# Kernel optimization log

Measured on AMD Instinct MI355X. Metric: run time of the kernel, lower is better.

The kernel has to match this reference:

```python
import jax, jax.numpy as jnp
import numpy as np

B, S, T, H, VS, VT = 64, 64, 64, 1024, 32000, 32000


def _init(key, shape, scale=0.05):
    return scale * jax.random.normal(key, shape, dtype=jnp.float32)


def setup_inputs() -> dict:
    key = jax.random.key(0)
    ks = jax.random.split(key, 16)
    source = jax.random.randint(ks[0], (B, S), 0, VS)
    target = jax.random.randint(ks[1], (B, T), 0, VT)
    emb_src = _init(ks[2], (VS, H)).at[0].set(0.0)   # padding_idx=0
    emb_tgt = _init(ks[3], (VT, H)).at[0].set(0.0)   # padding_idx=0
    W_ih_enc = _init(ks[4], (4 * H, H)); W_hh_enc = _init(ks[5], (4 * H, H))
    b_ih_enc = _init(ks[6], (4 * H,));   b_hh_enc = _init(ks[7], (4 * H,))
    W_ih_dec = _init(ks[8], (4 * H, H)); W_hh_dec = _init(ks[9], (4 * H, H))
    b_ih_dec = _init(ks[10], (4 * H,));  b_hh_dec = _init(ks[11], (4 * H,))
    W_att = _init(ks[12], (H, 2 * H));   b_att = _init(ks[13], (H,))
    W_out = _init(ks[14], (VT, H));      b_out = _init(ks[15], (VT,))
    return dict(source=source, target=target, emb_src=emb_src, emb_tgt=emb_tgt,
                W_ih_enc=W_ih_enc, W_hh_enc=W_hh_enc, b_ih_enc=b_ih_enc, b_hh_enc=b_hh_enc,
                W_ih_dec=W_ih_dec, W_hh_dec=W_hh_dec, b_ih_dec=b_ih_dec, b_hh_dec=b_hh_dec,
                W_att=W_att, b_att=b_att, W_out=W_out, b_out=b_out)


def _lstm_cell(x, h, c, W_ih, W_hh, b):
    # PyTorch gate order: i, f, g, o
    gates = x @ W_ih.T + h @ W_hh.T + b
    i, f, g, o = jnp.split(gates, 4, axis=-1)
    c_new = jax.nn.sigmoid(f) * c + jax.nn.sigmoid(i) * jnp.tanh(g)
    h_new = jax.nn.sigmoid(o) * jnp.tanh(c_new)
    return h_new, c_new


def reference(source, target, emb_src, emb_tgt,
              W_ih_enc, W_hh_enc, b_ih_enc, b_hh_enc,
              W_ih_dec, W_hh_dec, b_ih_dec, b_hh_dec,
              W_att, b_att, W_out, b_out):
    src = source.T              # [S, B]
    tgt = target.T              # [T, B]
    h0 = jnp.zeros((B, H), jnp.float32)
    c0 = jnp.zeros((B, H), jnp.float32)

    # ---- Encoder: time-major LSTM via scan (dropout in eval mode = identity) ----
    x_src = emb_src[src]        # [S, B, H]
    b_enc = b_ih_enc + b_hh_enc

    def enc_step(carry, x_t):
        h, c = carry
        h, c = _lstm_cell(x_t, h, c, W_ih_enc, W_hh_enc, b_enc)
        return (h, c), h

    (hT, cT), hx_list = jax.lax.scan(enc_step, (h0, c0), x_src)  # hx_list: [S, B, H]

    # ---- Decoder: hx_cx is never updated in the original loop, so every
    # timestep uses the SAME encoder final state -> fully vectorizable over t ----
    words_f = tgt[: S - 1]      # [Td, B], Td = T-1 (S == T)
    words_t = tgt[1:]           # [Td, B]
    x_dec = emb_tgt[words_f]    # [Td, B, H]
    b_dec = b_ih_dec + b_hh_dec
    gates = x_dec @ W_ih_dec.T + (hT @ W_hh_dec.T + b_dec)[None]  # [Td, B, 4H]
    i, f, g, o = jnp.split(gates, 4, axis=-1)
    c_new = jax.nn.sigmoid(f) * cT[None] + jax.nn.sigmoid(i) * jnp.tanh(g)
    hx = jax.nn.sigmoid(o) * jnp.tanh(c_new)                       # [Td, B, H]

    # ---- Attention (dot-product over source positions, softmax over S) ----
    scores = jnp.einsum('tbh,sbh->tsb', hx, hx_list)               # [Td, S, B]
    neg_inf = jnp.asarray(-jnp.inf, jnp.float32)
    mask = (src != 0)[None]                                        # [1, S, B]
    scores = jnp.where(mask, scores, neg_inf)
    align = jax.nn.softmax(scores, axis=1)                         # over S
    content = jnp.einsum('tsb,sbh->tbh', align, hx_list)           # [Td, B, H]
    concat = jnp.concatenate([content, hx], axis=-1)               # [Td, B, 2H]
    hx_att = jnp.tanh(concat @ W_att.T + b_att)                    # [Td, B, H]

    # ---- Output projection + per-step cross entropy (ignore_index=0), summed ----
    logits = hx_att @ W_out.T + b_out                              # [Td, B, VT]
    logp = jax.nn.log_softmax(logits, axis=-1)
    nll = -jnp.take_along_axis(logp, words_t[..., None], axis=-1).squeeze(-1)  # [Td, B]
    valid = (words_t != 0).astype(jnp.float32)
    per_step = jnp.sum(nll * valid, axis=1) / jnp.maximum(jnp.sum(valid, axis=1), 1.0)
    return jnp.sum(per_step)
```

## Files before the change

### kernel.cpp

```cpp
#include <hip/hip_runtime.h>
#include <math.h>

#define Bb 64
#define Ss 64
#define Hh 1024
#define Vv 32000
#define RD 4032
#define RP 4096
#define NT4 4096
#define ENC_NBLK 64

typedef unsigned short u16;
typedef unsigned long long u64;
typedef __attribute__((ext_vector_type(8))) short bf16x8;
typedef __attribute__((ext_vector_type(4))) float f32x4;

#define MFMA(a, b, c) __builtin_amdgcn_mfma_f32_16x16x32_bf16(a, b, c, 0, 0, 0)

__device__ __forceinline__ u16 f2b(float f) {
  union { float f; unsigned u; } v; v.f = f;
  unsigned r = v.u + 0x7fffu + ((v.u >> 16) & 1u);
  return (u16)(r >> 16);
}
__device__ __forceinline__ float b2f(u16 b) {
  union { unsigned u; float f; } v; v.u = ((unsigned)b) << 16; return v.f;
}
__device__ __forceinline__ float sigf(float x) { return 1.f / (1.f + expf(-x)); }

__device__ __forceinline__ u64 AL(const u64* p) {
  return __hip_atomic_load(p, __ATOMIC_RELAXED, __HIP_MEMORY_SCOPE_AGENT);
}
__device__ __forceinline__ void AS(u64* p, u64 v) {
  __hip_atomic_store(p, v, __ATOMIC_RELAXED, __HIP_MEMORY_SCOPE_AGENT);
}
__device__ __forceinline__ int AL32(const int* p) {
  return __hip_atomic_load(p, __ATOMIC_RELAXED, __HIP_MEMORY_SCOPE_AGENT);
}
__device__ __forceinline__ void AS32(int* p, int v) {
  __hip_atomic_store(p, v, __ATOMIC_RELAXED, __HIP_MEMORY_SCOPE_AGENT);
}

__device__ __forceinline__ void gll16(const void* g, void* l) {
  __builtin_amdgcn_global_load_lds(
      (const __attribute__((address_space(1))) unsigned int*)g,
      (__attribute__((address_space(3))) unsigned int*)l, 16, 0, 0);
}

__global__ void k_fail(float* out) { out[0] = 1e30f; }

__global__ void k_cvt_all(const float* __restrict__ s0, u16* __restrict__ d0,
                          const float* __restrict__ s1, u16* __restrict__ d1,
                          const float* __restrict__ s2, u16* __restrict__ d2,
                          const float* __restrict__ s3, u16* __restrict__ d3,
                          const float* __restrict__ s4, u16* __restrict__ d4,
                          const float* __restrict__ s5, u16* __restrict__ d5) {
  const int A4 = NT4 * Hh / 4;
  const int E4 = Hh * 2048 / 4;
  const int F4 = Vv * Hh / 4;
  const int TOT = 4 * A4 + E4 + F4;
  const int st = gridDim.x * blockDim.x;
  for (int i = blockIdx.x * blockDim.x + threadIdx.x; i < TOT; i += st) {
    const float* sp; u16* dp; int off;
    if (i < A4)            { sp = s0; dp = d0; off = i; }
    else if (i < 2 * A4)   { sp = s1; dp = d1; off = i - A4; }
    else if (i < 3 * A4)   { sp = s2; dp = d2; off = i - 2 * A4; }
    else if (i < 4 * A4)   { sp = s3; dp = d3; off = i - 3 * A4; }
    else if (i < 4 * A4 + E4) { sp = s4; dp = d4; off = i - 4 * A4; }
    else                   { sp = s5; dp = d5; off = i - 4 * A4 - E4; }
    const float4 v = ((const float4*)sp)[off];
    ushort4 o; o.x = f2b(v.x); o.y = f2b(v.y); o.z = f2b(v.z); o.w = f2b(v.w);
    ((ushort4*)dp)[off] = o;
  }
}

__global__ void k_gather2(const int* __restrict__ src_tok, const float* __restrict__ emb_s,
                          u16* __restrict__ out_s,
                          const int* __restrict__ tgt_tok, const float* __restrict__ emb_t,
                          u16* __restrict__ out_t) {
  int r = blockIdx.x;
  const int* tok; const float* emb; u16* outp; int nstep;
  if (r < RP) { tok = src_tok; emb = emb_s; outp = out_s; nstep = 64; }
  else        { r -= RP; tok = tgt_tok; emb = emb_t; outp = out_t; nstep = 63; }
  const int step = r >> 6, b = r & 63;
  const int idx = (step < nstep) ? tok[b * 64 + step] : 0;
  const float4 v = ((const float4*)(emb + (size_t)idx * Hh))[threadIdx.x];
  ushort4 o; o.x = f2b(v.x); o.y = f2b(v.y); o.z = f2b(v.z); o.w = f2b(v.w);
  ((ushort4*)(outp + (size_t)r * Hh))[threadIdx.x] = o;
}

__device__ __forceinline__ void dg_tile(const u16* __restrict__ A, const u16* __restrict__ Bm,
                                        u16* __restrict__ C, int bx, int by,
                                        u16* As, u16* Bs) {
  const int tid = threadIdx.x;
  const int wave = tid >> 6, lane = tid & 63;
  const int l15 = lane & 15, lhi = lane >> 4;
  const int m0 = by * 128, n0 = bx * 128;
  const int wm = (wave >> 1) * 64, wn = (wave & 1) * 64;
  f32x4 acc[4][4] = {};
  const int srow = wave * 32 + (lane >> 3);
  const int scolb = (lane & 7) * 16;
  for (int k0 = 0; k0 < Hh; k0 += 64) {
    __syncthreads();
#pragma unroll
    for (int q = 0; q < 4; ++q) {
      const int r = srow + q * 8;
      gll16((const char*)(A + (size_t)(m0 + r) * Hh + k0) + scolb,
            (char*)As + (wave * 32 + q * 8) * 128);
      gll16((const char*)(Bm + (size_t)(n0 + r) * Hh + k0) + scolb,
            (char*)Bs + (wave * 32 + q * 8) * 128);
    }
    __syncthreads();
#pragma unroll
    for (int kk = 0; kk < 2; ++kk) {
      const int ko = kk * 32 + lhi * 8;
      bf16x8 af[4], bfr[4];
#pragma unroll
      for (int i = 0; i < 4; ++i) af[i] = *(const bf16x8*)(As + (wm + i * 16 + l15) * 64 + ko);
#pragma unroll
      for (int j = 0; j < 4; ++j) bfr[j] = *(const bf16x8*)(Bs + (wn + j * 16 + l15) * 64 + ko);
#pragma unroll
      for (int i = 0; i < 4; ++i)
#pragma unroll
        for (int j = 0; j < 4; ++j)
          acc[i][j] = MFMA(af[i], bfr[j], acc[i][j]);
    }
  }
#pragma unroll
  for (int i = 0; i < 4; ++i) {
    const int gr = m0 + wm + i * 16 + lhi * 4;
#pragma unroll
    for (int j = 0; j < 4; ++j) {
      const int gc = n0 + wn + j * 16 + l15;
#pragma unroll
      for (int rr = 0; rr < 4; ++rr)
        C[(size_t)(gr + rr) * NT4 + gc] = f2b(acc[i][j][rr]);
    }
  }
}

__global__ __launch_bounds__(256)
void k_pre2(const u16* __restrict__ Ae, const u16* __restrict__ Be, u16* __restrict__ Ce,
            const u16* __restrict__ Ad, const u16* __restrict__ Bd, u16* __restrict__ Cd) {
  __shared__ __align__(16) u16 As[128 * 64];
  __shared__ __align__(16) u16 Bs[128 * 64];
  int t = blockIdx.x;
  if (t < 1024) dg_tile(Ae, Be, Ce, t & 31, t >> 5, As, Bs);
  else { t -= 1024; dg_tile(Ad, Bd, Cd, t & 31, t >> 5, As, Bs); }
}

template<int EPI>
__global__ __launch_bounds__(256)
void k_gemm(const u16* __restrict__ A, const u16* __restrict__ Bm,
            void* __restrict__ C, int M, int N, int K,
            const float* __restrict__ bias,
            float* __restrict__ pmax, float* __restrict__ psum, int ncols) {
  __shared__ __align__(16) u16 As[128 * 64];
  __shared__ __align__(16) u16 Bs[128 * 64];
  const int tid = threadIdx.x;
  const int wave = tid >> 6, lane = tid & 63;
  const int l15 = lane & 15, lhi = lane >> 4;
  int bx = blockIdx.x, by = blockIdx.y;
  {
    const int gx_ = gridDim.x, gy_ = gridDim.y;
    const int nwg = gx_ * gy_;
    if ((gy_ & 3) == 0 && (gx_ & 1) == 0) {
      const int f = by * gx_ + bx;
      const int x = f & 7, i = f >> 3;
      const int rby = gy_ >> 2, hx = gx_ >> 1;
      by = (x >> 1) * rby + (i % rby);
      bx = (x & 1) * hx + (i / rby);
    } else if ((nwg & 7) == 0) {
      int flat = by * gx_ + bx;
      const int qq = nwg >> 3;
      flat = (flat & 7) * qq + (flat >> 3);
      bx = flat % gx_; by = flat / gx_;
    }
  }
  const int m0 = by * 128, n0 = bx * 128;
  const int wm = (wave >> 1) * 64, wn = (wave & 1) * 64;
  f32x4 acc[4][4] = {};
  const int srow = wave * 32 + (lane >> 3);
  const int scolb = (lane & 7) * 16;

  for (int k0 = 0; k0 < K; k0 += 64) {
    __syncthreads();
#pragma unroll
    for (int q = 0; q < 4; ++q) {
      const int r = srow + q * 8;
      int ra = m0 + r; ra = (ra < M) ? ra : (M - 1);
      gll16((const char*)(A + (size_t)ra * K + k0) + scolb,
            (char*)As + (wave * 32 + q * 8) * 128);
      gll16((const char*)(Bm + (size_t)(n0 + r) * K + k0) + scolb,
            (char*)Bs + (wave * 32 + q * 8) * 128);
    }
    __syncthreads();
#pragma unroll
    for (int kk = 0; kk < 2; ++kk) {
      const int ko = kk * 32 + lhi * 8;
      bf16x8 af[4], bfr[4];
#pragma unroll
      for (int i = 0; i < 4; ++i) af[i] = *(const bf16x8*)(As + (wm + i * 16 + l15) * 64 + ko);
#pragma unroll
      for (int j = 0; j < 4; ++j) bfr[j] = *(const bf16x8*)(Bs + (wn + j * 16 + l15) * 64 + ko);
#pragma unroll
      for (int i = 0; i < 4; ++i)
#pragma unroll
        for (int j = 0; j < 4; ++j)
          acc[i][j] = MFMA(af[i], bfr[j], acc[i][j]);
    }
  }

  if (EPI == 0) {
#pragma unroll
    for (int i = 0; i < 4; ++i) {
      const int gr = m0 + wm + i * 16 + lhi * 4;
#pragma unroll
      for (int j = 0; j < 4; ++j) {
        const int gc = n0 + wn + j * 16 + l15;
        const float bv = bias ? bias[gc] : 0.f;
#pragma unroll
        for (int rr = 0; rr < 4; ++rr)
          ((float*)C)[(size_t)(gr + rr) * N + gc] = acc[i][j][rr] + bv;
      }
    }
  } else if (EPI == 3) {
#pragma unroll
    for (int i = 0; i < 4; ++i) {
      const int gr = m0 + wm + i * 16 + lhi * 4;
#pragma unroll
      for (int j = 0; j < 4; ++j) {
        const int gc = n0 + wn + j * 16 + l15;
        const float bv = bias[gc];
#pragma unroll
        for (int rr = 0; rr < 4; ++rr)
          ((u16*)C)[(size_t)(gr + rr) * N + gc] = f2b(tanhf(acc[i][j][rr] + bv));
      }
    }
  } else {
    float bj[4];
#pragma unroll
    for (int j = 0; j < 4; ++j) bj[j] = bias[n0 + wn + j * 16 + l15];
    const int pc = bx * 2 + (wn ? 1 : 0);
#pragma unroll
    for (int i = 0; i < 4; ++i) {
#pragma unroll
      for (int rr = 0; rr < 4; ++rr) {
        float v0 = acc[i][0][rr] + bj[0];
        float v1 = acc[i][1][rr] + bj[1];
        float v2 = acc[i][2][rr] + bj[2];
        float v3 = acc[i][3][rr] + bj[3];
        float m = fmaxf(fmaxf(v0, v1), fmaxf(v2, v3));
#pragma unroll
        for (int d = 1; d < 16; d <<= 1) m = fmaxf(m, __shfl_xor(m, d, 64));
        float s = __expf(v0 - m) + __expf(v1 - m) + __expf(v2 - m) + __expf(v3 - m);
#pragma unroll
        for (int d = 1; d < 16; d <<= 1) s += __shfl_xor(s, d, 64);
        if (l15 == 0) {
          const int grow = m0 + wm + i * 16 + lhi * 4 + rr;
          pmax[(size_t)grow * ncols + pc] = m;
          psum[(size_t)grow * ncols + pc] = s;
        }
      }
    }
  }
}

__global__ __launch_bounds__(256, 1)
void k_enc_all(const u16* __restrict__ Wb, const u16* __restrict__ gx,
               const float* __restrict__ b_ih, const float* __restrict__ b_hh,
               u16* __restrict__ hxl, float* __restrict__ c_out, int* flags) {
  __shared__ __align__(16) u16 Ws[64 * 1024];
  __shared__ float Gs[64 * 65];
  __shared__ float bsum[64];
  const int tid = threadIdx.x;
  const int wave = tid >> 6, lane = tid & 63;
  const int l15 = lane & 15, lhi = lane >> 4;
  const int c0 = blockIdx.x * 16;
  const int cb = tid >> 2, cq = tid & 3;
  const int rot = blockIdx.x & 31;

  for (int i = tid; i < 64 * 128; i += 256) {
    const int r = i >> 7, ck = i & 127;
    const int grow = (r >> 4) * Hh + c0 + (r & 15);
    const int bo = (ck * 16) ^ ((r & 7) << 4);
    *(bf16x8*)((char*)Ws + r * 2048 + bo) = *(const bf16x8*)(Wb + (size_t)grow * Hh + ck * 8);
  }
  if (tid < 64) {
    const int col = (tid >> 4) * Hh + c0 + (tid & 15);
    bsum[tid] = b_ih[col] + b_hh[col];
  }
  float creg[4] = {0.f, 0.f, 0.f, 0.f};
  __syncthreads();

  for (int s = 0; s < 64; ++s) {
    u64 graw[4];
#pragma unroll
    for (int g = 0; g < 4; ++g)
      graw[g] = *(const u64*)(gx + (size_t)(s * 64 + cb) * NT4 + g * Hh + c0 + cq * 4);

    f32x4 acc[4] = {};
    if (s > 0) {
      if (wave == 0) {
        for (;;) {
          const int f = AL32(flags + blockIdx.x * 64 + lane);
          if (__all(f >= s)) break;
          __builtin_amdgcn_s_sleep(1);
        }
      }
      __syncthreads();
      const u64* apw = (const u64*)(hxl + ((size_t)(s - 1) * 64 + wave * 16 + l15) * Hh);
      const char* wsb = (const char*)Ws;
      const int xr = (l15 & 7) << 4;
#pragma unroll 8
      for (int i = 0; i < 32; ++i) {
        const int kf = (i + rot) & 31;
        const int k = kf * 32 + lhi * 8;
        const u64 ua = AL(apw + (k >> 2));
        const u64 ub = AL(apw + (k >> 2) + 1);
        union { u64 qq[2]; bf16x8 v; } cv;
        cv.qq[0] = ua; cv.qq[1] = ub;
        const int kb = (k * 2) ^ xr;
#pragma unroll
        for (int nt = 0; nt < 4; ++nt)
          acc[nt] = MFMA(cv.v, *(const bf16x8*)(wsb + (nt * 16 + l15) * 2048 + kb), acc[nt]);
      }
    }
#pragma unroll
    for (int nt = 0; nt < 4; ++nt)
#pragma unroll
      for (int r = 0; r < 4; ++r)
        Gs[(wave * 16 + lhi * 4 + r) * 65 + nt * 16 + l15] = acc[nt][r];
    __syncthreads();
    {
      const float* gsrow = Gs + cb * 65;
      u64 pk = 0;
#pragma unroll
      for (int j = 0; j < 4; ++j) {
        const int col = cq * 4 + j;
        const float gi = gsrow[col]      + b2f((u16)(graw[0] >> (16 * j))) + bsum[col];
        const float gf = gsrow[16 + col] + b2f((u16)(graw[1] >> (16 * j))) + bsum[16 + col];
        const float gg = gsrow[32 + col] + b2f((u16)(graw[2] >> (16 * j))) + bsum[32 + col];
        const float go = gsrow[48 + col] + b2f((u16)(graw[3] >> (16 * j))) + bsum[48 + col];
        const float cn = sigf(gf) * creg[j] + sigf(gi) * tanhf(gg);
        const float hv = sigf(go) * tanhf(cn);
        creg[j] = cn;
        pk |= (u64)f2b(hv) << (16 * j);
      }
      AS((u64*)(hxl + ((size_t)s * 64 + cb) * Hh + c0 + cq * 4), pk);
    }
    __syncthreads();
    if (tid < ENC_NBLK)
      AS32(flags + tid * 64 + blockIdx.x, s + 1);
  }
#pragma unroll
  for (int j = 0; j < 4; ++j)
    c_out[cb * Hh + c0 + cq * 4 + j] = creg[j];
}

__global__ void k_dec_cell(const u16* __restrict__ G, const float* __restrict__ dbase,
                           const float* __restrict__ cT, const float* __restrict__ b_ih,
                           const float* __restrict__ b_hh, u16* __restrict__ Acat) {
  const int idx = blockIdx.x * 256 + threadIdx.x;
  const int r = idx >> 8, c4 = (idx & 255) * 4;
  if (r >= RD) return;
  const int b = r & 63;
  u64 graw[4]; f32x4 dv[4], bi[4], bh[4];
#pragma unroll
  for (int g = 0; g < 4; ++g) {
    graw[g] = *(const u64*)(G + (size_t)r * NT4 + g * Hh + c4);
    dv[g] = *(const f32x4*)(dbase + (size_t)b * NT4 + g * Hh + c4);
    bi[g] = *(const f32x4*)(b_ih + g * Hh + c4);
    bh[g] = *(const f32x4*)(b_hh + g * Hh + c4);
  }
  const f32x4 cv4 = *(const f32x4*)(cT + b * Hh + c4);
  u64 pk = 0;
#pragma unroll
  for (int j = 0; j < 4; ++j) {
    const float gi = b2f((u16)(graw[0] >> (16 * j))) + dv[0][j] + bi[0][j] + bh[0][j];
    const float gf = b2f((u16)(graw[1] >> (16 * j))) + dv[1][j] + bi[1][j] + bh[1][j];
    const float gg = b2f((u16)(graw[2] >> (16 * j))) + dv[2][j] + bi[2][j] + bh[2][j];
    const float go = b2f((u16)(graw[3] >> (16 * j))) + dv[3][j] + bi[3][j] + bh[3][j];
    const float cn = sigf(gf) * cv4[j] + sigf(gi) * tanhf(gg);
    const float hv = sigf(go) * tanhf(cn);
    pk |= (u64)f2b(hv) << (16 * j);
  }
  *(u64*)(Acat + (size_t)r * 2048 + Hh + c4) = pk;
}

__global__ __launch_bounds__(256)
void k_attn(u16* Acat, const u16* __restrict__ hxl, const int* __restrict__ src) {
  __shared__ float qs[Hh];
  __shared__ float sc[Ss];
  const int r = blockIdx.x;
  const int b = r & 63;
  const int tid = threadIdx.x, wave = tid >> 6, lane = tid & 63;
  for (int h = tid; h < Hh; h += 256) qs[h] = b2f(Acat[(size_t)r * 2048 + Hh + h]);
  __syncthreads();
  for (int sub = 0; sub < 16; ++sub) {
    const int ss = wave * 16 + sub;
    const ushort4* hp4 = (const ushort4*)(hxl + ((size_t)ss * Bb + b) * Hh);
    float p = 0.f;
#pragma unroll
    for (int q = 0; q < 4; ++q) {
      const int i4 = lane + 64 * q;
      const ushort4 v = hp4[i4];
      p += qs[i4 * 4 + 0] * b2f(v.x) + qs[i4 * 4 + 1] * b2f(v.y)
         + qs[i4 * 4 + 2] * b2f(v.z) + qs[i4 * 4 + 3] * b2f(v.w);
    }
#pragma unroll
    for (int d = 1; d < 64; d <<= 1) p += __shfl_xor(p, d, 64);
    if (lane == 0) sc[ss] = (src[b * 64 + ss] != 0) ? p : -INFINITY;
  }
  __syncthreads();
  if (wave == 0) {
    const float v = sc[lane];
    float m = v;
#pragma unroll
    for (int d = 1; d < 64; d <<= 1) m = fmaxf(m, __shfl_xor(m, d, 64));
    const float e = __expf(v - m);
    float ssum = e;
#pragma unroll
    for (int d = 1; d < 64; d <<= 1) ssum += __shfl_xor(ssum, d, 64);
    sc[lane] = e / ssum;
  }
  __syncthreads();
  float4 a4 = {0.f, 0.f, 0.f, 0.f};
  for (int s2 = 0; s2 < 64; ++s2) {
    const float a = sc[s2];
    const ushort4 v = *(const ushort4*)(hxl + ((size_t)s2 * Bb + b) * Hh + tid * 4);
    a4.x += a * b2f(v.x); a4.y += a * b2f(v.y);
    a4.z += a * b2f(v.z); a4.w += a * b2f(v.w);
  }
  u16* dst = Acat + (size_t)r * 2048 + tid * 4;
  dst[0] = f2b(a4.x); dst[1] = f2b(a4.y); dst[2] = f2b(a4.z); dst[3] = f2b(a4.w);
}

__global__ void k_lsetl(const float* __restrict__ pmax, const float* __restrict__ psum,
                        const u16* __restrict__ hx_att_b, const int* __restrict__ target,
                        const float* __restrict__ W, const float* __restrict__ bo,
                        float* __restrict__ nll, int ncols) {
  const int r = blockIdx.x * 4 + (threadIdx.x >> 6);
  const int lane = threadIdx.x & 63;
  if (r >= RD) return;
  float m = -INFINITY;
  for (int i = lane; i < ncols; i += 64) m = fmaxf(m, pmax[(size_t)r * ncols + i]);
#pragma unroll
  for (int d = 1; d < 64; d <<= 1) m = fmaxf(m, __shfl_xor(m, d, 64));
  float s = 0.f;
  for (int i = lane; i < ncols; i += 64)
    s += psum[(size_t)r * ncols + i] * __expf(pmax[(size_t)r * ncols + i] - m);
#pragma unroll
  for (int d = 1; d < 64; d <<= 1) s += __shfl_xor(s, d, 64);
  const int t = r >> 6, b = r & 63;
  const int w = target[b * 64 + t + 1];
  const u16* a = hx_att_b + (size_t)r * Hh;
  const float* wr = W + (size_t)w * Hh;
  float p = 0.f;
  for (int h = lane; h < Hh; h += 64) p += b2f(a[h]) * wr[h];
#pragma unroll
  for (int d = 1; d < 64; d <<= 1) p += __shfl_xor(p, d, 64);
  if (lane == 0) nll[r] = (m + logf(s)) - (p + bo[w]);
}

__global__ void k_final(const float* __restrict__ nll, const int* __restrict__ target,
                        float* __restrict__ out) {
  const int t = threadIdx.x;
  float ps = 0.f;
  if (t < 63) {
    float sn = 0.f, cnt = 0.f;
    for (int b = 0; b < 64; ++b) {
      const int r = t * 64 + b;
      const int w = target[b * 64 + t + 1];
      if (w != 0) { sn += nll[r]; cnt += 1.f; }
    }
    ps = sn / fmaxf(cnt, 1.f);
  }
#pragma unroll
  for (int d = 1; d < 64; d <<= 1) ps += __shfl_xor(ps, d, 64);
  if (t == 0) out[0] = ps;
}

extern "C" void kernel_launch(void* const* d_in, const int* in_sizes, int n_in,
                              void* d_out, int out_size, void* d_ws, size_t ws_size,
                              hipStream_t stream) {
  const int*   source   = (const int*)d_in[0];
  const int*   target   = (const int*)d_in[1];
  const float* emb_src  = (const float*)d_in[2];
  const float* emb_tgt  = (const float*)d_in[3];
  const float* W_ih_enc = (const float*)d_in[4];
  const float* W_hh_enc = (const float*)d_in[5];
  const float* b_ih_enc = (const float*)d_in[6];
  const float* b_hh_enc = (const float*)d_in[7];
  const float* W_ih_dec = (const float*)d_in[8];
  const float* W_hh_dec = (const float*)d_in[9];
  const float* b_ih_dec = (const float*)d_in[10];
  const float* b_hh_dec = (const float*)d_in[11];
  const float* W_att    = (const float*)d_in[12];
  const float* b_att    = (const float*)d_in[13];
  const float* W_out    = (const float*)d_in[14];
  const float* b_out    = (const float*)d_in[15];
  float* out = (float*)d_out;

  char* base = (char*)d_ws;
  size_t off = 0;
  auto alloc = [&](size_t bytes) -> void* {
    void* r = base + off; off += (bytes + 255) & ~(size_t)255; return r;
  };
  u16*   wb_ih_enc = (u16*)alloc((size_t)NT4 * Hh * 2);
  u16*   wb_hh_enc = (u16*)alloc((size_t)NT4 * Hh * 2);
  u16*   wb_ih_dec = (u16*)alloc((size_t)NT4 * Hh * 2);
  u16*   wb_hh_dec = (u16*)alloc((size_t)NT4 * Hh * 2);
  u16*   wb_att    = (u16*)alloc((size_t)Hh * 2048 * 2);
  u16*   wb_out    = (u16*)alloc((size_t)Vv * Hh * 2);
  u16*   x_src_b   = (u16*)alloc((size_t)RP * Hh * 2);
  u16*   x_dec_b   = (u16*)alloc((size_t)RP * Hh * 2);
  u16*   gates16   = (u16*)alloc((size_t)RP * NT4 * 2);
  u16*   gates_dec = (u16*)alloc((size_t)RP * NT4 * 2);
  u16*   hxl       = (u16*)alloc((size_t)Ss * Bb * Hh * 2);
  float* c_enc     = (float*)alloc((size_t)Bb * Hh * 4);
  float* dbase     = (float*)alloc((size_t)128 * NT4 * 4);
  u16*   Acat      = (u16*)alloc((size_t)RP * 2048 * 2);
  u16*   hx_att_b  = (u16*)alloc((size_t)RP * Hh * 2);
  float* pmax      = (float*)alloc((size_t)RP * 500 * 4);
  float* psum      = (float*)alloc((size_t)RP * 500 * 4);
  float* nll       = (float*)alloc((size_t)RD * 4);
  int*   flags     = (int*)alloc(ENC_NBLK * ENC_NBLK * 4);

  if (off > ws_size) { k_fail<<<1, 1, 0, stream>>>(out); return; }

  k_cvt_all<<<2048, 256, 0, stream>>>(W_ih_enc, wb_ih_enc, W_hh_enc, wb_hh_enc,
                                      W_ih_dec, wb_ih_dec, W_hh_dec, wb_hh_dec,
                                      W_att, wb_att, W_out, wb_out);

  hipMemsetAsync(flags, 0, ENC_NBLK * ENC_NBLK * 4, stream);

  k_gather2<<<2 * RP, 256, 0, stream>>>(source, emb_src, x_src_b,
                                        target, emb_tgt, x_dec_b);

  k_pre2<<<2048, 256, 0, stream>>>(x_src_b, wb_ih_enc, gates16,
                                   x_dec_b, wb_ih_dec, gates_dec);

  k_enc_all<<<ENC_NBLK, 256, 0, stream>>>(wb_hh_enc, gates16, b_ih_enc, b_hh_enc,
                                          hxl, c_enc, flags);

  k_gemm<0><<<dim3(32, 1), 256, 0, stream>>>(hxl + (size_t)63 * Bb * Hh, wb_hh_dec, dbase,
                                             64, NT4, Hh, nullptr, nullptr, nullptr, 0);
  k_dec_cell<<<RD, 256, 0, stream>>>(gates_dec, dbase, c_enc, b_ih_dec, b_hh_dec, Acat);

  k_attn<<<RD, 256, 0, stream>>>(Acat, hxl, source);

  k_gemm<3><<<dim3(8, 32), 256, 0, stream>>>(Acat, wb_att, hx_att_b, RP, Hh, 2048,
                                             b_att, nullptr, nullptr, 0);

  k_gemm<2><<<dim3(250, 32), 256, 0, stream>>>(hx_att_b, wb_out, nullptr, RP, Vv, Hh,
                                               b_out, pmax, psum, 500);
  k_lsetl<<<(RD + 3) / 4, 256, 0, stream>>>(pmax, psum, hx_att_b, target, W_out, b_out,
                                            nll, 500);
  k_final<<<1, 64, 0, stream>>>(nll, target, out);
}
```

Before: 1.506 ms.

## Add dedicated 256x256 double-buffered vocab GEMM with fused softmax partials

Replaces the generic 128x128 GEMM used for the 4096x32000 vocab projection with a specialised kernel. It uses 512 threads, 256x256 tiles and 128KB of LDS double buffering, with quarter-phase interleaving of global-to-LDS loads and MFMA plus s_setprio scheduling. Block IDs are swizzled so the 8-way block interleave covers contiguous tile ranges. The goal is more reuse per loaded byte and overlap of memory with compute in the dominant GEMM. The generic kernel also drops its grid swizzle, which can change L2 locality for the remaining GEMMs, and the 128KB LDS footprint limits occupancy.

```diff
diff --git a/kernel.cpp b/kernel.cpp
--- a/kernel.cpp
+++ b/kernel.cpp
@@ -152,30 +152,13 @@
 __global__ __launch_bounds__(256)
 void k_gemm(const u16* __restrict__ A, const u16* __restrict__ Bm,
             void* __restrict__ C, int M, int N, int K,
-            const float* __restrict__ bias,
-            float* __restrict__ pmax, float* __restrict__ psum, int ncols) {
+            const float* __restrict__ bias) {
   __shared__ __align__(16) u16 As[128 * 64];
   __shared__ __align__(16) u16 Bs[128 * 64];
   const int tid = threadIdx.x;
   const int wave = tid >> 6, lane = tid & 63;
   const int l15 = lane & 15, lhi = lane >> 4;
   int bx = blockIdx.x, by = blockIdx.y;
-  {
-    const int gx_ = gridDim.x, gy_ = gridDim.y;
-    const int nwg = gx_ * gy_;
-    if ((gy_ & 3) == 0 && (gx_ & 1) == 0) {
-      const int f = by * gx_ + bx;
-      const int x = f & 7, i = f >> 3;
-      const int rby = gy_ >> 2, hx = gx_ >> 1;
-      by = (x >> 1) * rby + (i % rby);
-      bx = (x & 1) * hx + (i / rby);
-    } else if ((nwg & 7) == 0) {
-      int flat = by * gx_ + bx;
-      const int qq = nwg >> 3;
-      flat = (flat & 7) * qq + (flat >> 3);
-      bx = flat % gx_; by = flat / gx_;
-    }
-  }
   const int m0 = by * 128, n0 = bx * 128;
   const int wm = (wave >> 1) * 64, wn = (wave & 1) * 64;
   f32x4 acc[4][4] = {};
@@ -223,7 +206,7 @@
           ((float*)C)[(size_t)(gr + rr) * N + gc] = acc[i][j][rr] + bv;
       }
     }
-  } else if (EPI == 3) {
+  } else {
 #pragma unroll
     for (int i = 0; i < 4; ++i) {
       const int gr = m0 + wm + i * 16 + lhi * 4;
@@ -236,30 +219,134 @@
           ((u16*)C)[(size_t)(gr + rr) * N + gc] = f2b(tanhf(acc[i][j][rr] + bv));
       }
     }
-  } else {
-    float bj[4];
-#pragma unroll
-    for (int j = 0; j < 4; ++j) bj[j] = bias[n0 + wn + j * 16 + l15];
-    const int pc = bx * 2 + (wn ? 1 : 0);
-#pragma unroll
-    for (int i = 0; i < 4; ++i) {
-#pragma unroll
-      for (int rr = 0; rr < 4; ++rr) {
-        float v0 = acc[i][0][rr] + bj[0];
-        float v1 = acc[i][1][rr] + bj[1];
-        float v2 = acc[i][2][rr] + bj[2];
-        float v3 = acc[i][3][rr] + bj[3];
-        float m = fmaxf(fmaxf(v0, v1), fmaxf(v2, v3));
-#pragma unroll
-        for (int d = 1; d < 16; d <<= 1) m = fmaxf(m, __shfl_xor(m, d, 64));
-        float s = __expf(v0 - m) + __expf(v1 - m) + __expf(v2 - m) + __expf(v3 - m);
-#pragma unroll
-        for (int d = 1; d < 16; d <<= 1) s += __shfl_xor(s, d, 64);
-        if (l15 == 0) {
-          const int grow = m0 + wm + i * 16 + lhi * 4 + rr;
-          pmax[(size_t)grow * ncols + pc] = m;
-          psum[(size_t)grow * ncols + pc] = s;
-        }
+  }
+}
+
+__device__ __forceinline__ void stageHT(const u16* __restrict__ g, int grow0, int kcol,
+                                        char* lbase, int wave, int lane) {
+#pragma unroll
+  for (int j = 0; j < 2; ++j) {
+    const int chunk = wave * 2 + j;
+    const int row = chunk * 8 + (lane >> 3);
+    gll16((const char*)(g + (size_t)(grow0 + row) * Hh + kcol) + (lane & 7) * 16,
+          lbase + chunk * 1024);
+  }
+}
+
+__global__ __launch_bounds__(512, 2)
+void k_vgemm(const u16* __restrict__ A, const u16* __restrict__ Bm,
+             const float* __restrict__ bias,
+             float* __restrict__ pmax, float* __restrict__ psum) {
+  __shared__ __align__(16) char LB[131072];
+  const int tid = threadIdx.x;
+  const int wave = tid >> 6, lane = tid & 63;
+  const int l15 = lane & 15, lhi = lane >> 4;
+  const int wm = wave >> 2, wn = wave & 3;
+  const int bid = blockIdx.x;
+  const int si = (bid & 7) * 250 + (bid >> 3);
+  const int bx = si >> 4, by = si & 15;
+  const int m0 = by * 256, n0 = bx * 256;
+
+  f32x4 acc[8][4] = {};
+  bf16x8 br[4][2], ar[2][2];
+
+#define ABUF(t) (LB + ((t) & 1) * 65536)
+#define BBUF(t) (LB + ((t) & 1) * 65536 + 32768)
+  auto stA = [&](int t, int h) {
+    if (t < 16) stageHT(A, m0 + h * 128, t * 64, ABUF(t) + h * 16384, wave, lane);
+  };
+  auto stB = [&](int t, int h) {
+    if (t < 16) stageHT(Bm, n0 + h * 128, t * 64, BBUF(t) + h * 16384, wave, lane);
+  };
+
+  stA(0, 0); stA(0, 1); stB(0, 0); stB(0, 1); stB(1, 0); stB(1, 1);
+  asm volatile("s_waitcnt vmcnt(4)" ::: "memory");
+  __builtin_amdgcn_sched_barrier(0);
+  __builtin_amdgcn_s_barrier();
+
+  auto phase = [&](int t, int q, bool rb, int stmat, int stt, int sth) {
+    const char* ab = (const char*)ABUF(t);
+    const char* bb = (const char*)BBUF(t);
+    if (rb) {
+#pragma unroll
+      for (int nf = 0; nf < 4; ++nf)
+#pragma unroll
+        for (int kk = 0; kk < 2; ++kk)
+          br[nf][kk] = *(const bf16x8*)(bb + (wn * 64 + nf * 16 + l15) * 128 +
+                                        (kk * 32 + lhi * 8) * 2);
+    }
+#pragma unroll
+    for (int m2 = 0; m2 < 2; ++m2)
+#pragma unroll
+      for (int kk = 0; kk < 2; ++kk)
+        ar[m2][kk] = *(const bf16x8*)(ab + (wm * 128 + (q * 2 + m2) * 16 + l15) * 128 +
+                                      (kk * 32 + lhi * 8) * 2);
+    if (stmat == 0) stA(stt, sth); else stB(stt, sth);
+    __builtin_amdgcn_sched_barrier(0);
+    __builtin_amdgcn_s_barrier();
+    asm volatile("s_waitcnt lgkmcnt(0)" ::: "memory");
+    __builtin_amdgcn_sched_barrier(0);
+    __builtin_amdgcn_s_setprio(1);
+#pragma unroll
+    for (int m2 = 0; m2 < 2; ++m2)
+#pragma unroll
+      for (int nf = 0; nf < 4; ++nf)
+#pragma unroll
+        for (int kk = 0; kk < 2; ++kk)
+          acc[q * 2 + m2][nf] = MFMA(ar[m2][kk], br[nf][kk], acc[q * 2 + m2][nf]);
+    __builtin_amdgcn_s_setprio(0);
+    __builtin_amdgcn_sched_barrier(0);
+  };
+
+  for (int t = 0; t < 16; t += 2) {
+    phase(t, 0, true,  0, t + 1, 0);
+    __builtin_amdgcn_s_barrier();
+    phase(t, 1, false, 0, t + 1, 1);
+    __builtin_amdgcn_s_barrier();
+    phase(t, 2, false, 1, t + 2, 0);
+    __builtin_amdgcn_s_barrier();
+    phase(t, 3, false, 1, t + 2, 1);
+    if (t == 14) asm volatile("s_waitcnt vmcnt(0)" ::: "memory");
+    else         asm volatile("s_waitcnt vmcnt(4)" ::: "memory");
+    __builtin_amdgcn_sched_barrier(0);
+    __builtin_amdgcn_s_barrier();
+    phase(t + 1, 0, true,  0, t + 2, 0);
+    __builtin_amdgcn_s_barrier();
+    phase(t + 1, 1, false, 0, t + 2, 1);
+    __builtin_amdgcn_s_barrier();
+    phase(t + 1, 2, false, 1, t + 3, 0);
+    __builtin_amdgcn_s_barrier();
+    phase(t + 1, 3, false, 1, t + 3, 1);
+    if (t == 14) asm volatile("s_waitcnt vmcnt(0)" ::: "memory");
+    else         asm volatile("s_waitcnt vmcnt(4)" ::: "memory");
+    __builtin_amdgcn_sched_barrier(0);
+    __builtin_amdgcn_s_barrier();
+  }
+#undef ABUF
+#undef BBUF
+
+  const int pc = bx * 4 + wn;
+  float bj[4];
+#pragma unroll
+  for (int nf = 0; nf < 4; ++nf) bj[nf] = bias[n0 + wn * 64 + nf * 16 + l15];
+#pragma unroll
+  for (int mf = 0; mf < 8; ++mf) {
+#pragma unroll
+    for (int rr = 0; rr < 4; ++rr) {
+      float v0 = acc[mf][0][rr] + bj[0];
+      float v1 = acc[mf][1][rr] + bj[1];
+      float v2 = acc[mf][2][rr] + bj[2];
+      float v3 = acc[mf][3][rr] + bj[3];
+      float m = fmaxf(fmaxf(v0, v1), fmaxf(v2, v3));
+#pragma unroll
+      for (int d = 1; d < 16; d <<= 1) m = fmaxf(m, __shfl_xor(m, d, 64));
+      float s = __expf(v0 - m) + __expf(v1 - m) + __expf(v2 - m) + __expf(v3 - m);
+#pragma unroll
+      for (int d = 1; d < 16; d <<= 1) s += __shfl_xor(s, d, 64);
+      if (l15 == 0) {
+        const int gr = m0 + wm * 128 + mf * 16 + lhi * 4 + rr;
+        pmax[(size_t)gr * 500 + pc] = m;
+        psum[(size_t)gr * 500 + pc] = s;
       }
     }
   }
@@ -544,16 +631,14 @@
                                           hxl, c_enc, flags);
 
   k_gemm<0><<<dim3(32, 1), 256, 0, stream>>>(hxl + (size_t)63 * Bb * Hh, wb_hh_dec, dbase,
-                                             64, NT4, Hh, nullptr, nullptr, nullptr, 0);
+                                             64, NT4, Hh, nullptr);
   k_dec_cell<<<RD, 256, 0, stream>>>(gates_dec, dbase, c_enc, b_ih_dec, b_hh_dec, Acat);
 
   k_attn<<<RD, 256, 0, stream>>>(Acat, hxl, source);
 
-  k_gemm<3><<<dim3(8, 32), 256, 0, stream>>>(Acat, wb_att, hx_att_b, RP, Hh, 2048,
-                                             b_att, nullptr, nullptr, 0);
-
-  k_gemm<2><<<dim3(250, 32), 256, 0, stream>>>(hx_att_b, wb_out, nullptr, RP, Vv, Hh,
-                                               b_out, pmax, psum, 500);
+  k_gemm<3><<<dim3(8, 32), 256, 0, stream>>>(Acat, wb_att, hx_att_b, RP, Hh, 2048, b_att);
+
+  k_vgemm<<<2000, 512, 0, stream>>>(hx_att_b, wb_out, b_out, pmax, psum);
   k_lsetl<<<(RD + 3) / 4, 256, 0, stream>>>(pmax, psum, hx_att_b, target, W_out, b_out,
                                             nll, 500);
   k_final<<<1, 64, 0, stream>>>(nll, target, out);
```

After: 1.402 ms. 6.9% less time.
